# Optimization experiments

Measured on AMD Instinct MI355X. Metric: run time of the kernel, lower is better.

The kernel has to match this reference:

```python
import jax, jax.numpy as jnp
import numpy as np

N, E, H, ED = 20000, 320000, 256, 64  # nodes, edges, hidden_dim, edge_feature_dim


def setup_inputs() -> dict:
    key = jax.random.key(0)
    ks = jax.random.split(key, 12)

    def init_w(k, shape, fan_in):
        return (jax.random.normal(k, shape, jnp.float32) / np.sqrt(fan_in)).astype(jnp.float32)

    h = jax.random.normal(ks[0], (N, H), jnp.float32)
    edge_indices = jax.random.randint(ks[1], (2, E), 0, N, jnp.int32)
    edge_attr = jax.random.normal(ks[2], (E, ED), jnp.float32)

    din = 2 * H + ED  # edge_network input: [h[row], h[col], edge_attr]
    W1 = init_w(ks[3], (H, din), din)
    b1 = jnp.zeros((H,), jnp.float32)
    W2 = init_w(ks[4], (H, H), H)
    b2 = jnp.zeros((H,), jnp.float32)
    # GRUCell params, gate order (r, z, n) as in torch
    W_ih = init_w(ks[5], (3 * H, H), H)
    b_ih = jnp.zeros((3 * H,), jnp.float32)
    W_hh = init_w(ks[6], (3 * H, H), H)
    b_hh = jnp.zeros((3 * H,), jnp.float32)

    return {"h": h, "edge_indices": edge_indices, "edge_attr": edge_attr,
            "W1": W1, "b1": b1, "W2": W2, "b2": b2,
            "W_ih": W_ih, "b_ih": b_ih, "W_hh": W_hh, "b_hh": b_hh}


def reference(h, edge_indices, edge_attr, W1, b1, W2, b2, W_ih, b_ih, W_hh, b_hh):
    row, col = edge_indices[0], edge_indices[1]
    # message: edge_network MLP on [h[row], h[col], edge_attr]
    edge_in = jnp.concatenate([h[row], h[col], edge_attr], axis=-1)  # [E, 2H+ED]
    msg = jax.nn.relu(edge_in @ W1.T + b1) @ W2.T + b2               # [E, H]
    # scatter_add aggregation by destination node (row)
    agg = jax.ops.segment_sum(msg, row, num_segments=h.shape[0])     # [N, H]
    # GRUCell update: input=agg, hidden=h
    gx = agg @ W_ih.T + b_ih
    gh = h @ W_hh.T + b_hh
    xr, xz, xn = jnp.split(gx, 3, axis=-1)
    hr, hz, hn = jnp.split(gh, 3, axis=-1)
    r = jax.nn.sigmoid(xr + hr)
    z = jax.nn.sigmoid(xz + hz)
    n = jnp.tanh(xn + r * hn)
    h_new = (1.0 - z) * n + z * h
    return h_new  # dropout p=0.0 -> identity
```

## Files before the change

kernel.cpp:

```cpp
#include <hip/hip_runtime.h>
#include <math.h>

#define NN 20000
#define NE 320000
#define HD 256
#define EDIM 64
#define DIN 576
#define ASTRIDE 264

typedef __attribute__((ext_vector_type(4))) _Float16 h4;
typedef __attribute__((ext_vector_type(8))) _Float16 h8;
typedef __attribute__((ext_vector_type(4))) float f32x4;

__device__ _Float16 g_W1cf[16 * 2 * 64 * 8];
__device__ _Float16 g_W12f[32 * 8 * 64 * 8];
__device__ _Float16 g_Wrzf[32 * 16 * 64 * 8];
__device__ _Float16 g_Wnxf[16 * 8 * 64 * 8];
__device__ _Float16 g_Wnhf[16 * 8 * 64 * 8];
__device__ float    g_Wib2[768];
__device__ _Float16 g_pre[(size_t)NN * 512];
__device__ _Float16 g_hf[(size_t)NN * 256];
__device__ _Float16 g_S16[(size_t)NN * 256];
__device__ _Float16 g_msg[(size_t)NE * 256];
__device__ int      g_rowptr[NN + 1];
__device__ int      g_cursor[NN];
__device__ int      g_epos[NE];
__device__ int      g_pcol[NE];

__device__ __forceinline__ h4 f2h4(float4 v) {
  return (h4){(_Float16)v.x, (_Float16)v.y, (_Float16)v.z, (_Float16)v.w};
}
__device__ __forceinline__ h8 f2h8(float4 a, float4 b) {
  return (h8){(_Float16)a.x, (_Float16)a.y, (_Float16)a.z, (_Float16)a.w,
              (_Float16)b.x, (_Float16)b.y, (_Float16)b.z, (_Float16)b.w};
}

__global__ __launch_bounds__(256) void cvtfold_kernel(
    const float* __restrict__ W1, const float* __restrict__ W_hh,
    const float* __restrict__ W_ih, const float* __restrict__ W2,
    const float* __restrict__ b2)
{
  const int bid = blockIdx.x;
  if (bid < 768) {
    const int r = bid, c = threadIdx.x;
    const float* wr = W_ih + (size_t)r * HD;
    float acc = 0.f;
    for (int m = 0; m < HD; ++m) acc += wr[m] * W2[(size_t)m * HD + c];
    const int ks = c >> 5, lg = (c >> 3) & 3, j = c & 7;
    const int l = lg * 16 + (r & 15);
    if (r < 512) {
      const int cf = (r < 256) ? (r >> 4) : (16 + ((r - 256) >> 4));
      g_Wrzf[(size_t)((cf * 16 + ks) * 64 + l) * 8 + j] = (_Float16)acc;
    } else {
      const int cf = (r - 512) >> 4;
      g_Wnxf[(size_t)((cf * 8 + ks) * 64 + l) * 8 + j] = (_Float16)acc;
    }
    if (c == 0) {
      float a2 = 0.f;
      for (int m = 0; m < HD; ++m) a2 += wr[m] * b2[m];
      g_Wib2[r] = a2;
    }
    return;
  }
  const int idx = (bid - 768) * 256 + threadIdx.x;
  const int g = idx >> 6, l = idx & 63;
  const int r16 = l & 15, koff = (l >> 4) * 8;
  const float* src; _Float16* dst;
  if (g < 32) {
    const int cf = g >> 1, ks = g & 1;
    src = &W1[(size_t)(cf * 16 + r16) * DIN + 512 + ks * 32 + koff];
    dst = &g_W1cf[(size_t)(cf * 2 + ks) * 512 + l * 8];
  } else if (g < 288) {
    const int gg = g - 32, cf = gg >> 3, ks = gg & 7;
    src = (cf < 16) ? &W1[(size_t)(cf * 16 + r16) * DIN + ks * 32 + koff]
                    : &W1[(size_t)((cf - 16) * 16 + r16) * DIN + 256 + ks * 32 + koff];
    dst = &g_W12f[(size_t)(cf * 8 + ks) * 512 + l * 8];
  } else if (g < 544) {
    const int gg = g - 288, cf = gg >> 3, ks = 8 + (gg & 7);
    const int row = (cf < 16) ? cf * 16 + r16 : 256 + (cf - 16) * 16 + r16;
    src = &W_hh[(size_t)row * HD + (ks - 8) * 32 + koff];
    dst = &g_Wrzf[(size_t)(cf * 16 + ks) * 512 + l * 8];
  } else {
    const int gg = g - 544, cf = gg >> 3, ks = gg & 7;
    src = &W_hh[(size_t)(512 + cf * 16 + r16) * HD + ks * 32 + koff];
    dst = &g_Wnhf[(size_t)(cf * 8 + ks) * 512 + l * 8];
  }
#pragma unroll
  for (int j = 0; j < 8; ++j) dst[j] = (_Float16)src[j];
}

#define PSTR 264
__global__ __launch_bounds__(256, 4) void pre_kernel(const float* __restrict__ h,
                                                     const int* __restrict__ ei,
                                                     int* __restrict__ deg) {
  __shared__ _Float16 A[32 * PSTR];
  const int t = threadIdx.x, w = t >> 6, l = t & 63;
  const int l15 = l & 15, lg = l >> 4;
  const int nb = blockIdx.x * 32;

  {
    const int gid = blockIdx.x * 256 + t;
    atomicAdd(&deg[ei[gid]], 1);
    atomicAdd(&deg[ei[gid + NE / 2]], 1);
  }

  const int row = t >> 3, c8 = t & 7;
#pragma unroll
  for (int i = 0; i < 8; ++i) {
    const int col4 = c8 + i * 8;
    float4 v = ((const float4*)(h + (size_t)(nb + row) * HD))[col4];
    const h4 x = f2h4(v);
    *(h4*)&A[row * PSTR + col4 * 4] = x;
    *(h4*)&g_hf[(size_t)(nb + row) * 256 + col4 * 4] = x;
  }
  __syncthreads();

  f32x4 acc[2][8];
#pragma unroll
  for (int m = 0; m < 2; ++m)
#pragma unroll
    for (int n = 0; n < 8; ++n) acc[m][n] = (f32x4){0.f, 0.f, 0.f, 0.f};

  for (int ks = 0; ks < 8; ++ks) {
    h8 a[2];
#pragma unroll
    for (int m = 0; m < 2; ++m)
      a[m] = *(const h8*)&A[(m * 16 + l15) * PSTR + ks * 32 + lg * 8];
#pragma unroll
    for (int n = 0; n < 8; ++n) {
      const h8 b = *(const h8*)&g_W12f[(size_t)((w * 8 + n) * 8 + ks) * 512 + l * 8];
#pragma unroll
      for (int m = 0; m < 2; ++m)
        acc[m][n] = __builtin_amdgcn_mfma_f32_16x16x32_f16(a[m], b, acc[m][n], 0, 0, 0);
    }
  }

#pragma unroll
  for (int m = 0; m < 2; ++m)
#pragma unroll
    for (int n = 0; n < 8; ++n) {
      const int col = w * 128 + n * 16 + l15;
#pragma unroll
      for (int r = 0; r < 4; ++r)
        g_pre[(size_t)(nb + m * 16 + lg * 4 + r) * 512 + col] = (_Float16)acc[m][n][r];
    }
}

__global__ __launch_bounds__(512) void scan_kernel(const int* __restrict__ deg) {
  __shared__ int part[512];
  const int t = threadIdx.x;
  const int base = t * 40;
  int loc[40];
  int s = 0;
#pragma unroll
  for (int i = 0; i < 40; ++i) {
    const int idx = base + i;
    const int d = (idx < NN) ? deg[idx] : 0;
    loc[i] = s; s += d;
  }
  part[t] = s;
  __syncthreads();
  for (int off = 1; off < 512; off <<= 1) {
    const int v = (t >= off) ? part[t - off] : 0;
    __syncthreads();
    part[t] += v;
    __syncthreads();
  }
  const int pre = (t == 0) ? 0 : part[t - 1];
#pragma unroll
  for (int i = 0; i < 40; ++i) {
    const int idx = base + i;
    if (idx < NN) { const int v = pre + loc[i]; g_rowptr[idx] = v; g_cursor[idx] = v; }
  }
  if (t == 511) g_rowptr[NN] = part[511];
}

__global__ __launch_bounds__(256) void scatter_kernel(const int* __restrict__ ei) {
  const int e = blockIdx.x * 256 + threadIdx.x;
  if (e < NE) {
    const int p = atomicAdd(&g_cursor[ei[e]], 1);
    g_epos[e] = p;
    g_pcol[p] = ei[NE + e];
  }
}

__global__ __launch_bounds__(256) void msg_kernel(const float* __restrict__ eattr) {
  __shared__ _Float16 T[64 * ASTRIDE];
  const int t = threadIdx.x, w = t >> 6, l = t & 63;
  const int l15 = l & 15, lg = l >> 4;
  const int e0 = blockIdx.x * 64;

  f32x4 acc[4][4];
#pragma unroll
  for (int m = 0; m < 4; ++m)
#pragma unroll
    for (int n = 0; n < 4; ++n) acc[m][n] = (f32x4){0.f, 0.f, 0.f, 0.f};

#pragma unroll
  for (int ks = 0; ks < 2; ++ks) {
    h8 a[4], b[4];
#pragma unroll
    for (int m = 0; m < 4; ++m) {
      const float* ep = eattr + (size_t)(e0 + m * 16 + l15) * EDIM + ks * 32 + lg * 8;
      a[m] = f2h8(((const float4*)ep)[0], ((const float4*)ep)[1]);
    }
#pragma unroll
    for (int n = 0; n < 4; ++n)
      b[n] = *(const h8*)&g_W1cf[(size_t)((w * 4 + n) * 2 + ks) * 512 + l * 8];
#pragma unroll
    for (int m = 0; m < 4; ++m)
#pragma unroll
      for (int n = 0; n < 4; ++n)
        acc[m][n] = __builtin_amdgcn_mfma_f32_16x16x32_f16(a[m], b[n], acc[m][n], 0, 0, 0);
  }

#pragma unroll
  for (int m = 0; m < 4; ++m)
#pragma unroll
    for (int n = 0; n < 4; ++n)
#pragma unroll
      for (int r = 0; r < 4; ++r)
        T[(m * 16 + lg * 4 + r) * ASTRIDE + w * 64 + n * 16 + l15] = (_Float16)acc[m][n][r];
  __syncthreads();

#pragma unroll
  for (int i = 0; i < 16; ++i) {
    const int e = w * 16 + i;
    const int p = g_epos[e0 + e];
    *(h4*)&g_msg[(size_t)p * 256 + l * 4] = *(const h4*)&T[e * ASTRIDE + l * 4];
  }
}

__global__ __launch_bounds__(256) void agg_kernel(const float* __restrict__ b1) {
  const int t = threadIdx.x, w = t >> 6, l = t & 63;
  const int n = blockIdx.x * 4 + w;
  const int start = g_rowptr[n];
  const int end = g_rowptr[n + 1];

  const h4 p1 = *(const h4*)&g_pre[(size_t)n * 512 + l * 4];
  const f32x4 b1v = *(const f32x4*)&b1[l * 4];
  f32x4 base;
#pragma unroll
  for (int r = 0; r < 4; ++r) base[r] = (float)p1[r] + b1v[r];

  f32x4 acc = (f32x4){0.f, 0.f, 0.f, 0.f};
  int p = start;
  for (; p + 4 <= end; p += 4) {
    h4 m[4], q[4];
#pragma unroll
    for (int k = 0; k < 4; ++k) {
      m[k] = *(const h4*)&g_msg[(size_t)(p + k) * 256 + l * 4];
      q[k] = *(const h4*)&g_pre[(size_t)g_pcol[p + k] * 512 + 256 + l * 4];
    }
#pragma unroll
    for (int k = 0; k < 4; ++k)
#pragma unroll
      for (int r = 0; r < 4; ++r) {
        float v = base[r] + (float)m[k][r] + (float)q[k][r];
        acc[r] += v > 0.f ? v : 0.f;
      }
  }
  for (; p < end; ++p) {
    const h4 m0 = *(const h4*)&g_msg[(size_t)p * 256 + l * 4];
    const h4 q0 = *(const h4*)&g_pre[(size_t)g_pcol[p] * 512 + 256 + l * 4];
#pragma unroll
    for (int r = 0; r < 4; ++r) {
      float v = base[r] + (float)m0[r] + (float)q0[r];
      acc[r] += v > 0.f ? v : 0.f;
    }
  }
  *(h4*)&g_S16[(size_t)n * 256 + l * 4] =
      (h4){(_Float16)acc[0], (_Float16)acc[1], (_Float16)acc[2], (_Float16)acc[3]};
}

__global__ __launch_bounds__(256, 2) void node_kernel(
    const float* __restrict__ b_ih, const float* __restrict__ b_hh,
    float* __restrict__ out)
{
  const int bid = blockIdx.x;
  const int cf = bid & 3, rng = bid >> 2;
  const int t = threadIdx.x, w = t >> 6, l = t & 63;
  const int l15 = l & 15, lg = l >> 4;
  const int nb = rng * 64;
  const int cf0 = cf * 4;
  int na = nb + w * 16 + l15; if (na >= NN) na = NN - 1;

  f32x4 ar[4], az[4], ax[4], ah[4];
#pragma unroll
  for (int n = 0; n < 4; ++n) {
    ar[n] = (f32x4){0.f, 0.f, 0.f, 0.f}; az[n] = (f32x4){0.f, 0.f, 0.f, 0.f};
    ax[n] = (f32x4){0.f, 0.f, 0.f, 0.f}; ah[n] = (f32x4){0.f, 0.f, 0.f, 0.f};
  }

  const _Float16* aS = &g_S16[(size_t)na * 256 + lg * 8];
  const _Float16* aH = &g_hf[(size_t)na * 256 + lg * 8];

#pragma unroll
  for (int ks = 0; ks < 8; ++ks) {
    const h8 a = *(const h8*)&aS[ks * 32];
    h8 br[4], bz[4], bn[4];
#pragma unroll
    for (int n = 0; n < 4; ++n) {
      br[n] = *(const h8*)&g_Wrzf[(size_t)(((cf0 + n) * 16 + ks) * 64 + l) * 8];
      bz[n] = *(const h8*)&g_Wrzf[(size_t)(((16 + cf0 + n) * 16 + ks) * 64 + l) * 8];
      bn[n] = *(const h8*)&g_Wnxf[(size_t)(((cf0 + n) * 8 + ks) * 64 + l) * 8];
    }
#pragma unroll
    for (int n = 0; n < 4; ++n) {
      ar[n] = __builtin_amdgcn_mfma_f32_16x16x32_f16(a, br[n], ar[n], 0, 0, 0);
      az[n] = __builtin_amdgcn_mfma_f32_16x16x32_f16(a, bz[n], az[n], 0, 0, 0);
      ax[n] = __builtin_amdgcn_mfma_f32_16x16x32_f16(a, bn[n], ax[n], 0, 0, 0);
    }
  }

#pragma unroll
  for (int ks = 0; ks < 8; ++ks) {
    const h8 a = *(const h8*)&aH[ks * 32];
    h8 br[4], bz[4], bn[4];
#pragma unroll
    for (int n = 0; n < 4; ++n) {
      br[n] = *(const h8*)&g_Wrzf[(size_t)(((cf0 + n) * 16 + 8 + ks) * 64 + l) * 8];
      bz[n] = *(const h8*)&g_Wrzf[(size_t)(((16 + cf0 + n) * 16 + 8 + ks) * 64 + l) * 8];
      bn[n] = *(const h8*)&g_Wnhf[(size_t)(((cf0 + n) * 8 + ks) * 64 + l) * 8];
    }
#pragma unroll
    for (int n = 0; n < 4; ++n) {
      ar[n] = __builtin_amdgcn_mfma_f32_16x16x32_f16(a, br[n], ar[n], 0, 0, 0);
      az[n] = __builtin_amdgcn_mfma_f32_16x16x32_f16(a, bz[n], az[n], 0, 0, 0);
      ah[n] = __builtin_amdgcn_mfma_f32_16x16x32_f16(a, bn[n], ah[n], 0, 0, 0);
    }
  }

#pragma unroll
  for (int r = 0; r < 4; ++r) {
    const int node = nb + w * 16 + lg * 4 + r;
    if (node >= NN) continue;
    const float df = (float)(g_rowptr[node + 1] - g_rowptr[node]);
#pragma unroll
    for (int n = 0; n < 4; ++n) {
      const int c = cf * 64 + n * 16 + l15;
      const float rg = 1.f / (1.f + __expf(-(ar[n][r] + df * g_Wib2[c] + b_ih[c] + b_hh[c])));
      const float zg = 1.f / (1.f + __expf(-(az[n][r] + df * g_Wib2[HD + c] + b_ih[HD + c] + b_hh[HD + c])));
      const float u  = ax[n][r] + df * g_Wib2[2 * HD + c] + b_ih[2 * HD + c]
                       + rg * (ah[n][r] + b_hh[2 * HD + c]);
      const float eu = __expf(2.f * fabsf(u));
      const float ng = copysignf(1.f - 2.f / (eu + 1.f), u);
      const float hv = (float)g_hf[(size_t)node * 256 + c];
      out[(size_t)node * HD + c] = (1.f - zg) * ng + zg * hv;
    }
  }
}

extern "C" void kernel_launch(void* const* d_in, const int* in_sizes, int n_in,
                              void* d_out, int out_size, void* d_ws, size_t ws_size,
                              hipStream_t stream)
{
  const float* h     = (const float*)d_in[0];
  const int*   ei    = (const int*)d_in[1];
  const float* eattr = (const float*)d_in[2];
  const float* W1    = (const float*)d_in[3];
  const float* b1    = (const float*)d_in[4];
  const float* W2    = (const float*)d_in[5];
  const float* b2    = (const float*)d_in[6];
  const float* W_ih  = (const float*)d_in[7];
  const float* b_ih  = (const float*)d_in[8];
  const float* W_hh  = (const float*)d_in[9];
  const float* b_hh  = (const float*)d_in[10];
  float* out = (float*)d_out;

  int* deg = (int*)d_ws;

  hipMemsetAsync(deg, 0, (size_t)NN * 4, stream);
  cvtfold_kernel<<<768 + 168, 256, 0, stream>>>(W1, W_hh, W_ih, W2, b2);
  pre_kernel<<<NN / 32, 256, 0, stream>>>(h, ei, deg);
  scan_kernel<<<1, 512, 0, stream>>>(deg);
  scatter_kernel<<<(NE + 255) / 256, 256, 0, stream>>>(ei);
  msg_kernel<<<NE / 64, 256, 0, stream>>>(eattr);
  agg_kernel<<<NN / 4, 256, 0, stream>>>(b1);
  node_kernel<<<1252, 256, 0, stream>>>(b_ih, b_hh, out);
}
```

Before: 298.3 us.

## Fuse message and aggregation kernels via sorted-edge processing with atomic accumulation

Measured after the change: 326.1 us. +9.3%, slower.

```diff
diff --git a/kernel.cpp b/kernel.cpp
--- a/kernel.cpp
+++ b/kernel.cpp
@@ -20,11 +20,10 @@
 __device__ float    g_Wib2[768];
 __device__ _Float16 g_pre[(size_t)NN * 512];
 __device__ _Float16 g_hf[(size_t)NN * 256];
-__device__ _Float16 g_S16[(size_t)NN * 256];
-__device__ _Float16 g_msg[(size_t)NE * 256];
 __device__ int      g_rowptr[NN + 1];
 __device__ int      g_cursor[NN];
-__device__ int      g_epos[NE];
+__device__ int      g_perm[NE];
+__device__ int      g_prow[NE];
 __device__ int      g_pcol[NE];
 
 __device__ __forceinline__ h4 f2h4(float4 v) {
@@ -178,17 +177,25 @@
 __global__ __launch_bounds__(256) void scatter_kernel(const int* __restrict__ ei) {
   const int e = blockIdx.x * 256 + threadIdx.x;
   if (e < NE) {
-    const int p = atomicAdd(&g_cursor[ei[e]], 1);
-    g_epos[e] = p;
+    const int r = ei[e];
+    const int p = atomicAdd(&g_cursor[r], 1);
+    g_perm[p] = e;
+    g_prow[p] = r;
     g_pcol[p] = ei[NE + e];
   }
 }
 
-__global__ __launch_bounds__(256) void msg_kernel(const float* __restrict__ eattr) {
+__global__ __launch_bounds__(256, 4) void aggmsg_kernel(const float* __restrict__ eattr,
+                                                        const float* __restrict__ b1,
+                                                        float* __restrict__ S32) {
   __shared__ _Float16 T[64 * ASTRIDE];
   const int t = threadIdx.x, w = t >> 6, l = t & 63;
   const int l15 = l & 15, lg = l >> 4;
-  const int e0 = blockIdx.x * 64;
+  const int p0 = blockIdx.x * 64;
+
+  int pe[4];
+#pragma unroll
+  for (int m = 0; m < 4; ++m) pe[m] = g_perm[p0 + m * 16 + l15];
 
   f32x4 acc[4][4];
 #pragma unroll
@@ -201,7 +208,7 @@
     h8 a[4], b[4];
 #pragma unroll
     for (int m = 0; m < 4; ++m) {
-      const float* ep = eattr + (size_t)(e0 + m * 16 + l15) * EDIM + ks * 32 + lg * 8;
+      const float* ep = eattr + (size_t)pe[m] * EDIM + ks * 32 + lg * 8;
       a[m] = f2h8(((const float4*)ep)[0], ((const float4*)ep)[1]);
     }
 #pragma unroll
@@ -223,57 +230,40 @@
         T[(m * 16 + lg * 4 + r) * ASTRIDE + w * 64 + n * 16 + l15] = (_Float16)acc[m][n][r];
   __syncthreads();
 
+  const f32x4 b1v = *(const f32x4*)&b1[l * 4];
+  int cur = -1;
+  f32x4 sum = (f32x4){0.f, 0.f, 0.f, 0.f};
 #pragma unroll
   for (int i = 0; i < 16; ++i) {
-    const int e = w * 16 + i;
-    const int p = g_epos[e0 + e];
-    *(h4*)&g_msg[(size_t)p * 256 + l * 4] = *(const h4*)&T[e * ASTRIDE + l * 4];
-  }
-}
-
-__global__ __launch_bounds__(256) void agg_kernel(const float* __restrict__ b1) {
-  const int t = threadIdx.x, w = t >> 6, l = t & 63;
-  const int n = blockIdx.x * 4 + w;
-  const int start = g_rowptr[n];
-  const int end = g_rowptr[n + 1];
-
-  const h4 p1 = *(const h4*)&g_pre[(size_t)n * 512 + l * 4];
-  const f32x4 b1v = *(const f32x4*)&b1[l * 4];
-  f32x4 base;
-#pragma unroll
-  for (int r = 0; r < 4; ++r) base[r] = (float)p1[r] + b1v[r];
-
-  f32x4 acc = (f32x4){0.f, 0.f, 0.f, 0.f};
-  int p = start;
-  for (; p + 4 <= end; p += 4) {
-    h4 m[4], q[4];
-#pragma unroll
-    for (int k = 0; k < 4; ++k) {
-      m[k] = *(const h4*)&g_msg[(size_t)(p + k) * 256 + l * 4];
-      q[k] = *(const h4*)&g_pre[(size_t)g_pcol[p + k] * 512 + 256 + l * 4];
-    }
-#pragma unroll
-    for (int k = 0; k < 4; ++k)
-#pragma unroll
-      for (int r = 0; r < 4; ++r) {
-        float v = base[r] + (float)m[k][r] + (float)q[k][r];
-        acc[r] += v > 0.f ? v : 0.f;
+    const int p = p0 + w * 16 + i;
+    const int node = g_prow[p];
+    const int src  = g_pcol[p];
+    const h4 tt = *(const h4*)&T[(w * 16 + i) * ASTRIDE + l * 4];
+    const h4 q1 = *(const h4*)&g_pre[(size_t)node * 512 + l * 4];
+    const h4 q2 = *(const h4*)&g_pre[(size_t)src * 512 + 256 + l * 4];
+    f32x4 v;
+#pragma unroll
+    for (int r = 0; r < 4; ++r) {
+      float x = (float)tt[r] + (float)q1[r] + (float)q2[r] + b1v[r];
+      v[r] = x > 0.f ? x : 0.f;
+    }
+    if (node != cur) {
+      if (cur >= 0) {
+#pragma unroll
+        for (int r = 0; r < 4; ++r) unsafeAtomicAdd(&S32[(size_t)cur * HD + l * 4 + r], sum[r]);
       }
-  }
-  for (; p < end; ++p) {
-    const h4 m0 = *(const h4*)&g_msg[(size_t)p * 256 + l * 4];
-    const h4 q0 = *(const h4*)&g_pre[(size_t)g_pcol[p] * 512 + 256 + l * 4];
-#pragma unroll
-    for (int r = 0; r < 4; ++r) {
-      float v = base[r] + (float)m0[r] + (float)q0[r];
-      acc[r] += v > 0.f ? v : 0.f;
-    }
-  }
-  *(h4*)&g_S16[(size_t)n * 256 + l * 4] =
-      (h4){(_Float16)acc[0], (_Float16)acc[1], (_Float16)acc[2], (_Float16)acc[3]};
+      cur = node; sum = v;
+    } else {
+#pragma unroll
+      for (int r = 0; r < 4; ++r) sum[r] += v[r];
+    }
+  }
+#pragma unroll
+  for (int r = 0; r < 4; ++r) unsafeAtomicAdd(&S32[(size_t)cur * HD + l * 4 + r], sum[r]);
 }
 
 __global__ __launch_bounds__(256, 2) void node_kernel(
+    const float* __restrict__ S32,
     const float* __restrict__ b_ih, const float* __restrict__ b_hh,
     float* __restrict__ out)
 {
@@ -292,12 +282,14 @@
     ax[n] = (f32x4){0.f, 0.f, 0.f, 0.f}; ah[n] = (f32x4){0.f, 0.f, 0.f, 0.f};
   }
 
-  const _Float16* aS = &g_S16[(size_t)na * 256 + lg * 8];
+  const float* aS = &S32[(size_t)na * 256 + lg * 8];
   const _Float16* aH = &g_hf[(size_t)na * 256 + lg * 8];
 
 #pragma unroll
   for (int ks = 0; ks < 8; ++ks) {
-    const h8 a = *(const h8*)&aS[ks * 32];
+    const float4 s0 = ((const float4*)&aS[ks * 32])[0];
+    const float4 s1 = ((const float4*)&aS[ks * 32])[1];
+    const h8 a = f2h8(s0, s1);
     h8 br[4], bz[4], bn[4];
 #pragma unroll
     for (int n = 0; n < 4; ++n) {
@@ -368,14 +360,14 @@
   const float* b_hh  = (const float*)d_in[10];
   float* out = (float*)d_out;
 
-  int* deg = (int*)d_ws;
-
-  hipMemsetAsync(deg, 0, (size_t)NN * 4, stream);
+  float* S32 = (float*)d_ws;
+  int*   deg = (int*)((char*)d_ws + (size_t)NN * HD * 4);
+
+  hipMemsetAsync(d_ws, 0, (size_t)NN * HD * 4 + (size_t)NN * 4, stream);
   cvtfold_kernel<<<768 + 168, 256, 0, stream>>>(W1, W_hh, W_ih, W2, b2);
   pre_kernel<<<NN / 32, 256, 0, stream>>>(h, ei, deg);
   scan_kernel<<<1, 512, 0, stream>>>(deg);
   scatter_kernel<<<(NE + 255) / 256, 256, 0, stream>>>(ei);
-  msg_kernel<<<NE / 64, 256, 0, stream>>>(eattr);
-  agg_kernel<<<NN / 4, 256, 0, stream>>>(b1);
-  node_kernel<<<1252, 256, 0, stream>>>(b_ih, b_hh, out);
-}
+  aggmsg_kernel<<<NE / 64, 256, 0, stream>>>(eattr, b1, S32);
+  node_kernel<<<1252, 256, 0, stream>>>(S32, b_ih, b_hh, out);
+}
```

## Fuse edge scatter and ReLU pre-activation into msg kernel, simplify aggregation

Applied to the files above, without the earlier changes.

Measured after the change: 297.9 us. About the same (-0.1%).

```diff
diff --git a/kernel.cpp b/kernel.cpp
--- a/kernel.cpp
+++ b/kernel.cpp
@@ -24,8 +24,6 @@
 __device__ _Float16 g_msg[(size_t)NE * 256];
 __device__ int      g_rowptr[NN + 1];
 __device__ int      g_cursor[NN];
-__device__ int      g_epos[NE];
-__device__ int      g_pcol[NE];
 
 __device__ __forceinline__ h4 f2h4(float4 v) {
   return (h4){(_Float16)v.x, (_Float16)v.y, (_Float16)v.z, (_Float16)v.w};
@@ -175,21 +173,17 @@
   if (t == 511) g_rowptr[NN] = part[511];
 }
 
-__global__ __launch_bounds__(256) void scatter_kernel(const int* __restrict__ ei) {
-  const int e = blockIdx.x * 256 + threadIdx.x;
-  if (e < NE) {
-    const int p = atomicAdd(&g_cursor[ei[e]], 1);
-    g_epos[e] = p;
-    g_pcol[p] = ei[NE + e];
-  }
-}
-
-__global__ __launch_bounds__(256) void msg_kernel(const float* __restrict__ eattr) {
+__global__ __launch_bounds__(256, 4) void msg_kernel(const float* __restrict__ eattr,
+                                                     const int* __restrict__ ei,
+                                                     const float* __restrict__ b1) {
   __shared__ _Float16 T[64 * ASTRIDE];
+  __shared__ int pL[64];
   const int t = threadIdx.x, w = t >> 6, l = t & 63;
   const int l15 = l & 15, lg = l >> 4;
   const int e0 = blockIdx.x * 64;
 
+  if (t < 64) pL[t] = atomicAdd(&g_cursor[ei[e0 + t]], 1);
+
   f32x4 acc[4][4];
 #pragma unroll
   for (int m = 0; m < 4; ++m)
@@ -223,51 +217,48 @@
         T[(m * 16 + lg * 4 + r) * ASTRIDE + w * 64 + n * 16 + l15] = (_Float16)acc[m][n][r];
   __syncthreads();
 
+  const f32x4 b1v = *(const f32x4*)&b1[l * 4];
 #pragma unroll
   for (int i = 0; i < 16; ++i) {
     const int e = w * 16 + i;
-    const int p = g_epos[e0 + e];
-    *(h4*)&g_msg[(size_t)p * 256 + l * 4] = *(const h4*)&T[e * ASTRIDE + l * 4];
-  }
-}
-
-__global__ __launch_bounds__(256) void agg_kernel(const float* __restrict__ b1) {
+    const int ge = e0 + e;
+    const int dest = ei[ge];
+    const int srcn = ei[NE + ge];
+    const h4 tt = *(const h4*)&T[e * ASTRIDE + l * 4];
+    const h4 q1 = *(const h4*)&g_pre[(size_t)dest * 512 + l * 4];
+    const h4 q2 = *(const h4*)&g_pre[(size_t)srcn * 512 + 256 + l * 4];
+    h4 o;
+#pragma unroll
+    for (int r = 0; r < 4; ++r) {
+      float x = (float)tt[r] + (float)q1[r] + (float)q2[r] + b1v[r];
+      o[r] = (_Float16)(x > 0.f ? x : 0.f);
+    }
+    *(h4*)&g_msg[(size_t)pL[e] * 256 + l * 4] = o;
+  }
+}
+
+__global__ __launch_bounds__(256) void agg_kernel() {
   const int t = threadIdx.x, w = t >> 6, l = t & 63;
   const int n = blockIdx.x * 4 + w;
   const int start = g_rowptr[n];
   const int end = g_rowptr[n + 1];
 
-  const h4 p1 = *(const h4*)&g_pre[(size_t)n * 512 + l * 4];
-  const f32x4 b1v = *(const f32x4*)&b1[l * 4];
-  f32x4 base;
-#pragma unroll
-  for (int r = 0; r < 4; ++r) base[r] = (float)p1[r] + b1v[r];
-
   f32x4 acc = (f32x4){0.f, 0.f, 0.f, 0.f};
   int p = start;
   for (; p + 4 <= end; p += 4) {
-    h4 m[4], q[4];
-#pragma unroll
-    for (int k = 0; k < 4; ++k) {
+    h4 m[4];
+#pragma unroll
+    for (int k = 0; k < 4; ++k)
       m[k] = *(const h4*)&g_msg[(size_t)(p + k) * 256 + l * 4];
-      q[k] = *(const h4*)&g_pre[(size_t)g_pcol[p + k] * 512 + 256 + l * 4];
-    }
 #pragma unroll
     for (int k = 0; k < 4; ++k)
 #pragma unroll
-      for (int r = 0; r < 4; ++r) {
-        float v = base[r] + (float)m[k][r] + (float)q[k][r];
-        acc[r] += v > 0.f ? v : 0.f;
-      }
+      for (int r = 0; r < 4; ++r) acc[r] += (float)m[k][r];
   }
   for (; p < end; ++p) {
     const h4 m0 = *(const h4*)&g_msg[(size_t)p * 256 + l * 4];
-    const h4 q0 = *(const h4*)&g_pre[(size_t)g_pcol[p] * 512 + 256 + l * 4];
-#pragma unroll
-    for (int r = 0; r < 4; ++r) {
-      float v = base[r] + (float)m0[r] + (float)q0[r];
-      acc[r] += v > 0.f ? v : 0.f;
-    }
+#pragma unroll
+    for (int r = 0; r < 4; ++r) acc[r] += (float)m0[r];
   }
   *(h4*)&g_S16[(size_t)n * 256 + l * 4] =
       (h4){(_Float16)acc[0], (_Float16)acc[1], (_Float16)acc[2], (_Float16)acc[3]};
@@ -374,8 +365,7 @@
   cvtfold_kernel<<<768 + 168, 256, 0, stream>>>(W1, W_hh, W_ih, W2, b2);
   pre_kernel<<<NN / 32, 256, 0, stream>>>(h, ei, deg);
   scan_kernel<<<1, 512, 0, stream>>>(deg);
-  scatter_kernel<<<(NE + 255) / 256, 256, 0, stream>>>(ei);
-  msg_kernel<<<NE / 64, 256, 0, stream>>>(eattr);
-  agg_kernel<<<NN / 4, 256, 0, stream>>>(b1);
+  msg_kernel<<<NE / 64, 256, 0, stream>>>(eattr, ei, b1);
+  agg_kernel<<<NN / 4, 256, 0, stream>>>();
   node_kernel<<<1252, 256, 0, stream>>>(b_ih, b_hh, out);
 }
```
